# Performance work log

Hardware: AMD Instinct MI355X
Metric: run time of the kernel (lower is better)

The kernel has to match this reference:

```python
import jax, jax.numpy as jnp
import numpy as np

B, S, D_IN = 2, 2048, 1024
DIM, H, G = 64, 16, 4  # head dim, num_heads, kv groups


def setup_inputs() -> dict:
    key = jax.random.key(0)
    ks = jax.random.split(key, 9)
    query = jax.random.normal(ks[0], (B, S, D_IN), dtype=jnp.float32)
    key_t = jax.random.normal(ks[1], (B, S, D_IN), dtype=jnp.float32)
    value = jax.random.normal(ks[2], (B, S, D_IN), dtype=jnp.float32)
    # causal mask; masked_fill where mask == 0
    mask = jnp.tril(jnp.ones((S, S), dtype=jnp.int32))[None]  # [1,S,S]
    sc = 1.0 / np.sqrt(D_IN)
    Wq = jax.random.normal(ks[3], (H, D_IN, DIM), dtype=jnp.float32) * sc
    bq = jnp.zeros((H, DIM), dtype=jnp.float32)
    Wk = jax.random.normal(ks[4], (G, D_IN, DIM), dtype=jnp.float32) * sc
    bk = jnp.zeros((G, DIM), dtype=jnp.float32)
    Wv = jax.random.normal(ks[5], (G, D_IN, DIM), dtype=jnp.float32) * sc
    bv = jnp.zeros((G, DIM), dtype=jnp.float32)
    return {"query": query, "key": key_t, "value": value, "mask": mask,
            "Wq": Wq, "bq": bq, "Wk": Wk, "bk": bk, "Wv": Wv, "bv": bv}


def reference(query, key, value, mask, Wq, bq, Wk, bk, Wv, bv):
    # batched per-head projections (replaces the Python loop over heads)
    Q = jnp.einsum('bsd,hde->bhse', query, Wq) + bq[None, :, None, :]   # [B,H,S,E]
    K = jnp.einsum('bsd,gde->bgse', key, Wk) + bk[None, :, None, :]     # [B,G,S,E]
    V = jnp.einsum('bsd,gde->bgse', value, Wv) + bv[None, :, None, :]   # [B,G,S,E]
    # head i uses KV group i % G (as in the original loop)
    g_idx = jnp.arange(H) % G
    Kh = K[:, g_idx]  # [B,H,S,E]
    Vh = V[:, g_idx]
    attn = jnp.einsum('bhqe,bhke->bhqk', Q, Kh) / np.sqrt(DIM)          # [B,H,S,S]
    attn = jnp.where(mask[:, None] == 0, jnp.float32(-1e9), attn)
    p = jax.nn.softmax(attn, axis=-1)
    z = jnp.einsum('bhqk,bhke->bhqe', p, Vh)                             # [B,H,S,E]
    # concat heads along last dim (same order as torch.cat of z_list)
    return z.transpose(0, 2, 1, 3).reshape(B, S, H * DIM)
```

## Files before the change

### kernel.cpp

```cpp
#include <hip/hip_runtime.h>
#include <hip/hip_bf16.h>
#include <math.h>

#define S_LEN 2048
#define DIN   1024
#define NH    16
#define NG    4

typedef short s16x8 __attribute__((ext_vector_type(8)));
typedef float f32x4 __attribute__((ext_vector_type(4)));

__device__ __forceinline__ unsigned short f2bf(float x) {
  union { float f; unsigned u; } v; v.f = x;
  unsigned r = v.u + 0x7FFFu + ((v.u >> 16) & 1u);
  return (unsigned short)(r >> 16);
}
__device__ __forceinline__ unsigned cvtpk(float a, float b) {
  unsigned r;
  asm("v_cvt_pk_bf16_f32 %0, %1, %2" : "=v"(r) : "v"(a), "v"(b));
  return r;
}


__global__ __launch_bounds__(256) void k_cast(
    const float* __restrict__ q, const float* __restrict__ k,
    const float* __restrict__ v, unsigned short* __restrict__ AF) {
  const float* src = (blockIdx.y == 0) ? q : (blockIdx.y == 1) ? k : v;
  unsigned short* dst = AF + (size_t)blockIdx.y * 4194304;
  int flat = blockIdx.x * 256 + threadIdx.x;
  int b = flat >> 18, s = (flat >> 7) & 2047, d0 = (flat & 127) * 8;
  const float* sp = src + (size_t)(b * 2048 + s) * 1024 + d0;
  float4 x = *(const float4*)sp;
  float4 y = *(const float4*)(sp + 4);
  union { s16x8 v; unsigned u[4]; } r;
  r.u[0] = cvtpk(x.x, x.y); r.u[1] = cvtpk(x.z, x.w);
  r.u[2] = cvtpk(y.x, y.y); r.u[3] = cvtpk(y.z, y.w);
  unsigned short* p = dst + (size_t)((b * 128 + (s >> 4)) * 32 + (d0 >> 5)) * 512
                    + (s & 15) * 8 + ((d0 >> 3) & 3) * 128;
  *(s16x8*)p = r.v;
}

__global__ __launch_bounds__(256) void k_wtrans(
    const float* __restrict__ Wq, const float* __restrict__ Wk,
    const float* __restrict__ Wv, unsigned short* __restrict__ WF) {
  __shared__ __align__(16) unsigned short T[64][72];
  const int u = blockIdx.x >> 4, D0 = (blockIdx.x & 15) * 64;
  const int t = threadIdx.x;
  const float* src = (u < 16) ? (Wq + (size_t)u * 65536)
                   : (u < 20) ? (Wk + (size_t)(u - 16) * 65536)
                              : (Wv + (size_t)(u - 20) * 65536);
  const int e4 = (t & 15) * 4, dl = t >> 4;
  #pragma unroll
  for (int p = 0; p < 4; ++p) {
    const int d = p * 16 + dl;
    float4 v = *(const float4*)(src + (size_t)(D0 + d) * 64 + e4);
    T[e4 + 0][d] = f2bf(v.x); T[e4 + 1][d] = f2bf(v.y);
    T[e4 + 2][d] = f2bf(v.z); T[e4 + 3][d] = f2bf(v.w);
  }
  __syncthreads();
  const int j = t & 7;
  #pragma unroll
  for (int p = 0; p < 2; ++p) {
    const int e = p * 32 + (t >> 3);
    unsigned short* dst = WF + (size_t)u * 65536
        + (size_t)((e >> 4) * 32 + (D0 >> 5) + (j >> 2)) * 512
        + (e & 15) * 8 + (j & 3) * 128;
    *(s16x8*)dst = *(const s16x8*)&T[e][j * 8];
  }
}

__global__ __launch_bounds__(256, 4) void k_project(
    const unsigned short* __restrict__ AF,
    const float* __restrict__ bq, const float* __restrict__ bk,
    const float* __restrict__ bv,
    const unsigned short* __restrict__ WF,
    unsigned short* __restrict__ QF,
    unsigned short* __restrict__ KF,
    unsigned short* __restrict__ VF) {
  const int i = blockIdx.x;
  const int lid = (i & 7) * 96 + (i >> 3);
  const int strip = lid / 48;
  const int rr = lid % 48;
  const int b = rr / 24, u = rr % 24;
  const int tid = threadIdx.x;
  const int w = tid >> 6, lane = tid & 63, lq = lane & 15, gq = lane >> 4;

  const unsigned short* AFp = AF
      + (size_t)((u < 16) ? 0 : (u < 20) ? 1 : 2) * 4194304
      + (size_t)b * 2097152;
  const float* bias = (u < 16) ? bq + u * 64
                    : (u < 20) ? bk + (u - 16) * 64 : bv + (u - 20) * 64;
  const unsigned short* WFp = WF + (size_t)u * 65536;
  const int sb0 = strip * 8 + w * 2;
  const float OSC = (u < 16) ? 0.1803368801111204f : 1.0f;

  f32x4 acc[2][4] = {};
  s16x8 aE[2], bE[4], aO[2], bO[4];

  auto LD = [&](s16x8 (&a)[2], s16x8 (&bf)[4], int dk) {
    a[0] = *(const s16x8*)(AFp + (size_t)((sb0 + 0) * 32 + dk) * 512 + lane * 8);
    a[1] = *(const s16x8*)(AFp + (size_t)((sb0 + 1) * 32 + dk) * 512 + lane * 8);
    #pragma unroll
    for (int n = 0; n < 4; ++n)
      bf[n] = *(const s16x8*)(WFp + (size_t)(n * 32 + dk) * 512 + lane * 8);
  };
  auto FM = [&](const s16x8 (&a)[2], const s16x8 (&bf)[4]) {
    #pragma unroll
    for (int rf = 0; rf < 2; ++rf)
      #pragma unroll
      for (int n = 0; n < 4; ++n)
        acc[rf][n] = __builtin_amdgcn_mfma_f32_16x16x32_bf16(a[rf], bf[n], acc[rf][n], 0, 0, 0);
  };

  LD(aE, bE, 0);
  for (int dk = 0; dk < 32; dk += 2) {
    LD(aO, bO, dk + 1);
    FM(aE, bE);
    if (dk + 2 < 32) LD(aE, bE, dk + 2);
    FM(aO, bO);
  }

  float bvv[4];
  #pragma unroll
  for (int n = 0; n < 4; ++n) bvv[n] = bias[n * 16 + lq];

  unsigned short* dst = (u < 16) ? QF + (size_t)(b * 16 + u) * 131072
                      : (u < 20) ? KF + (size_t)(b * 4 + (u - 16)) * 131072
                                 : VF + (size_t)(b * 4 + (u - 20)) * 131072;
  #pragma unroll
  for (int rf = 0; rf < 2; ++rf)
    #pragma unroll
    for (int n = 0; n < 4; ++n)
      #pragma unroll
      for (int r = 0; r < 4; ++r) {
        const int s = strip * 128 + w * 32 + rf * 16 + gq * 4 + r;
        const int d = n * 16 + lq;
        const unsigned short hv = f2bf((acc[rf][n][r] + bvv[n]) * OSC);
        if (u < 20)
          dst[(size_t)((s >> 4) * 2 + (d >> 5)) * 512
              + (s & 15) * 8 + ((d >> 3) & 3) * 128 + (d & 7)] = hv;
        else
          dst[(size_t)(n * 64 + (s >> 5)) * 512
              + lq * 8 + ((s >> 3) & 3) * 128 + (s & 7)] = hv;
      }
}

__global__ __launch_bounds__(256, 3) void k_attn(
    const unsigned short* __restrict__ QF, const unsigned short* __restrict__ KF,
    const unsigned short* __restrict__ VF, float* __restrict__ out) {
  __shared__ __align__(16) unsigned short P[4][16][72];
  const int tid = threadIdx.x;
  const int w = tid >> 6, lane = tid & 63, lq = lane & 15, gq = lane >> 4;
  const int x = blockIdx.x;
  const int xcd = x & 7, li = x >> 3;
  const int g = xcd & 3;
  const int j = 127 - (li * 2 + (xcd >> 2));
  const int h = g + 4 * w;
  const int b = blockIdx.y;

  const unsigned short* QFp = QF + (size_t)(b * NH + h) * 131072;
  const unsigned short* KFp = KF + (size_t)(b * NG + g) * 131072;
  const unsigned short* VFp = VF + (size_t)(b * NG + g) * 131072;
  const int nt = (j >> 2) + 1;

  const s16x8 qf0 = *(const s16x8*)(QFp + (size_t)(j * 2 + 0) * 512 + lane * 8);
  const s16x8 qf1 = *(const s16x8*)(QFp + (size_t)(j * 2 + 1) * 512 + lane * 8);
  f32x4 z[4] = {};
  float lsum = 0.f;

  auto loadK = [&](s16x8 (&A)[4], s16x8 (&B)[4], int t) {
    #pragma unroll
    for (int f = 0; f < 4; ++f) {
      const unsigned short* kp = KFp + (size_t)((t * 4 + f) * 2) * 512 + lane * 8;
      A[f] = *(const s16x8*)kp;
      B[f] = *(const s16x8*)(kp + 512);
    }
  };

  auto tile = [&](const s16x8 (&kA)[4], const s16x8 (&kB)[4], int t) {
    const int k0 = t * 64;
    s16x8 vb[4][2];
    #pragma unroll
    for (int n = 0; n < 4; ++n)
      #pragma unroll
      for (int ks = 0; ks < 2; ++ks)
        vb[n][ks] = *(const s16x8*)(VFp + (size_t)(n * 64 + t * 2 + ks) * 512 + lane * 8);
    f32x4 sv[4];
    __builtin_amdgcn_s_setprio(1);
    #pragma unroll
    for (int f = 0; f < 4; ++f) {
      f32x4 s = {};
      s = __builtin_amdgcn_mfma_f32_16x16x32_bf16(kA[f], qf0, s, 0, 0, 0);
      s = __builtin_amdgcn_mfma_f32_16x16x32_bf16(kB[f], qf1, s, 0, 0, 0);
      sv[f] = s;
    }
    __builtin_amdgcn_s_setprio(0);
    if (t == nt - 1) {
      const int qrow = j * 16 + lq;
      #pragma unroll
      for (int f = 0; f < 4; ++f)
        #pragma unroll
        for (int r = 0; r < 4; ++r)
          if (k0 + f * 16 + gq * 4 + r > qrow) sv[f][r] = -1e30f;
    }
    float s0 = 0.f, s1 = 0.f;
    #pragma unroll
    for (int f = 0; f < 4; ++f) {
      float p0 = __builtin_amdgcn_exp2f(sv[f][0]);
      float p1 = __builtin_amdgcn_exp2f(sv[f][1]);
      float p2 = __builtin_amdgcn_exp2f(sv[f][2]);
      float p3 = __builtin_amdgcn_exp2f(sv[f][3]);
      s0 += p0 + p1; s1 += p2 + p3;
      *(uint2*)&P[w][lq][f * 16 + gq * 4] = make_uint2(cvtpk(p0, p1), cvtpk(p2, p3));
    }
    lsum += s0 + s1;
    s16x8 pa[2];
    #pragma unroll
    for (int ks = 0; ks < 2; ++ks)
      pa[ks] = *(const s16x8*)&P[w][lq][ks * 32 + gq * 8];
    __builtin_amdgcn_s_setprio(1);
    #pragma unroll
    for (int n = 0; n < 4; ++n)
      #pragma unroll
      for (int ks = 0; ks < 2; ++ks)
        z[n] = __builtin_amdgcn_mfma_f32_16x16x32_bf16(pa[ks], vb[n][ks], z[n], 0, 0, 0);
    __builtin_amdgcn_s_setprio(0);
  };

  s16x8 cA[4], cB[4], nA[4], nB[4];
  loadK(cA, cB, 0);
  int t = 0;
  while (true) {
    loadK(nA, nB, (t + 1 < nt) ? t + 1 : t);
    tile(cA, cB, t);
    if (++t >= nt) break;
    loadK(cA, cB, (t + 1 < nt) ? t + 1 : t);
    tile(nA, nB, t);
    if (++t >= nt) break;
  }

  lsum += __shfl_xor(lsum, 16);
  lsum += __shfl_xor(lsum, 32);
  float* outp = out + (size_t)b * S_LEN * 1024 + h * 64;
  #pragma unroll
  for (int r = 0; r < 4; ++r) {
    float lr = __shfl(lsum, gq * 4 + r, 64);
    float inv = __builtin_amdgcn_rcpf(lr);
    float* op = outp + (size_t)(j * 16 + gq * 4 + r) * 1024;
    #pragma unroll
    for (int n = 0; n < 4; ++n) op[n * 16 + lq] = z[n][r] * inv;
  }
}

extern "C" void kernel_launch(void* const* d_in, const int* in_sizes, int n_in,
                              void* d_out, int out_size, void* d_ws, size_t ws_size,
                              hipStream_t stream) {
  const float* query = (const float*)d_in[0];
  const float* key   = (const float*)d_in[1];
  const float* value = (const float*)d_in[2];
  const float* Wq = (const float*)d_in[4];
  const float* bq = (const float*)d_in[5];
  const float* Wk = (const float*)d_in[6];
  const float* bk = (const float*)d_in[7];
  const float* Wv = (const float*)d_in[8];
  const float* bv = (const float*)d_in[9];
  float* out = (float*)d_out;

  unsigned short* AF = (unsigned short*)d_ws;
  unsigned short* WF = AF + 12582912;
  unsigned short* QF = WF + 1572864;
  unsigned short* KF = QF + 4194304;
  unsigned short* VF = KF + 1048576;

  hipLaunchKernelGGL(k_cast, dim3(2048, 3), dim3(256), 0, stream,
                     query, key, value, AF);
  hipLaunchKernelGGL(k_wtrans, dim3(384), dim3(256), 0, stream, Wq, Wk, Wv, WF);
  hipLaunchKernelGGL(k_project, dim3(768), dim3(256), 0, stream,
                     AF, bq, bk, bv, WF, QF, KF, VF);
  hipLaunchKernelGGL(k_attn, dim3(512, 2), dim3(256), 0, stream, QF, KF, VF, out);
}
```

Before: 90.92 us.

## Stage shared K/V tiles in LDS via global_load_lds double buffering

In the attention kernel, each of the four waves now loads a quarter of each K and V tile straight into a double-buffered shared-memory region with global_load_lds, instead of every wave fetching the full tiles into registers. The four heads in a block share one KV group, so this cuts redundant global and L2 traffic by four and frees the registers that held K/V. The cost is a block-wide barrier with vmcnt(0) on every tile, extra LDS reads, and dropping the occupancy hint from launch bounds.

```diff
diff --git a/kernel.cpp b/kernel.cpp
--- a/kernel.cpp
+++ b/kernel.cpp
@@ -20,6 +20,11 @@
   asm("v_cvt_pk_bf16_f32 %0, %1, %2" : "=v"(r) : "v"(a), "v"(b));
   return r;
 }
+
+#define GLOAD_LDS16(gsrc, ldst)                                              \
+  __builtin_amdgcn_global_load_lds(                                         \
+      (const __attribute__((address_space(1))) unsigned int*)(gsrc),        \
+      (__attribute__((address_space(3))) unsigned int*)(ldst), 16, 0, 0)
 
 
 __global__ __launch_bounds__(256) void k_cast(
@@ -145,9 +150,10 @@
       }
 }
 
-__global__ __launch_bounds__(256, 3) void k_attn(
+__global__ __launch_bounds__(256) void k_attn(
     const unsigned short* __restrict__ QF, const unsigned short* __restrict__ KF,
     const unsigned short* __restrict__ VF, float* __restrict__ out) {
+  __shared__ __align__(16) unsigned short KV[2][8192];
   __shared__ __align__(16) unsigned short P[4][16][72];
   const int tid = threadIdx.x;
   const int w = tid >> 6, lane = tid & 63, lq = lane & 15, gq = lane >> 4;
@@ -168,34 +174,34 @@
   f32x4 z[4] = {};
   float lsum = 0.f;
 
-  auto loadK = [&](s16x8 (&A)[4], s16x8 (&B)[4], int t) {
-    #pragma unroll
-    for (int f = 0; f < 4; ++f) {
-      const unsigned short* kp = KFp + (size_t)((t * 4 + f) * 2) * 512 + lane * 8;
-      A[f] = *(const s16x8*)kp;
-      B[f] = *(const s16x8*)(kp + 512);
-    }
-  };
-
-  auto tile = [&](const s16x8 (&kA)[4], const s16x8 (&kB)[4], int t) {
-    const int k0 = t * 64;
-    s16x8 vb[4][2];
-    #pragma unroll
-    for (int n = 0; n < 4; ++n)
-      #pragma unroll
-      for (int ks = 0; ks < 2; ++ks)
-        vb[n][ks] = *(const s16x8*)(VFp + (size_t)(n * 64 + t * 2 + ks) * 512 + lane * 8);
+  auto stage = [&](int t, int buf) {
+    const unsigned short* ks = KFp + (size_t)t * 4096 + (w * 2) * 512 + lane * 8;
+    unsigned short* kd = &KV[buf][(w * 2) * 512];
+    GLOAD_LDS16(ks, kd);
+    GLOAD_LDS16(ks + 512, kd + 512);
+    const unsigned short* vs = VFp + (size_t)(w * 64 + t * 2) * 512 + lane * 8;
+    unsigned short* vd = &KV[buf][4096 + (w * 2) * 512];
+    GLOAD_LDS16(vs, vd);
+    GLOAD_LDS16(vs + 512, vd + 512);
+  };
+
+  auto tile = [&](int t, int buf) {
+    const unsigned short* kb = &KV[buf][0];
+    const unsigned short* vb = &KV[buf][4096];
     f32x4 sv[4];
     __builtin_amdgcn_s_setprio(1);
     #pragma unroll
     for (int f = 0; f < 4; ++f) {
+      const s16x8 kA = *(const s16x8*)(kb + (f * 2 + 0) * 512 + lane * 8);
+      const s16x8 kB = *(const s16x8*)(kb + (f * 2 + 1) * 512 + lane * 8);
       f32x4 s = {};
-      s = __builtin_amdgcn_mfma_f32_16x16x32_bf16(kA[f], qf0, s, 0, 0, 0);
-      s = __builtin_amdgcn_mfma_f32_16x16x32_bf16(kB[f], qf1, s, 0, 0, 0);
+      s = __builtin_amdgcn_mfma_f32_16x16x32_bf16(kA, qf0, s, 0, 0, 0);
+      s = __builtin_amdgcn_mfma_f32_16x16x32_bf16(kB, qf1, s, 0, 0, 0);
       sv[f] = s;
     }
     __builtin_amdgcn_s_setprio(0);
     if (t == nt - 1) {
+      const int k0 = t * 64;
       const int qrow = j * 16 + lq;
       #pragma unroll
       for (int f = 0; f < 4; ++f)
@@ -214,29 +220,29 @@
       *(uint2*)&P[w][lq][f * 16 + gq * 4] = make_uint2(cvtpk(p0, p1), cvtpk(p2, p3));
     }
     lsum += s0 + s1;
-    s16x8 pa[2];
-    #pragma unroll
-    for (int ks = 0; ks < 2; ++ks)
-      pa[ks] = *(const s16x8*)&P[w][lq][ks * 32 + gq * 8];
+    const s16x8 pa0 = *(const s16x8*)&P[w][lq][gq * 8];
+    const s16x8 pa1 = *(const s16x8*)&P[w][lq][32 + gq * 8];
     __builtin_amdgcn_s_setprio(1);
     #pragma unroll
-    for (int n = 0; n < 4; ++n)
-      #pragma unroll
-      for (int ks = 0; ks < 2; ++ks)
-        z[n] = __builtin_amdgcn_mfma_f32_16x16x32_bf16(pa[ks], vb[n][ks], z[n], 0, 0, 0);
+    for (int n = 0; n < 4; ++n) {
+      const s16x8 v0 = *(const s16x8*)(vb + (n * 2 + 0) * 512 + lane * 8);
+      const s16x8 v1 = *(const s16x8*)(vb + (n * 2 + 1) * 512 + lane * 8);
+      z[n] = __builtin_amdgcn_mfma_f32_16x16x32_bf16(pa0, v0, z[n], 0, 0, 0);
+      z[n] = __builtin_amdgcn_mfma_f32_16x16x32_bf16(pa1, v1, z[n], 0, 0, 0);
+    }
     __builtin_amdgcn_s_setprio(0);
   };
 
-  s16x8 cA[4], cB[4], nA[4], nB[4];
-  loadK(cA, cB, 0);
-  int t = 0;
-  while (true) {
-    loadK(nA, nB, (t + 1 < nt) ? t + 1 : t);
-    tile(cA, cB, t);
-    if (++t >= nt) break;
-    loadK(cA, cB, (t + 1 < nt) ? t + 1 : t);
-    tile(nA, nB, t);
-    if (++t >= nt) break;
+  stage(0, 0);
+  asm volatile("s_waitcnt vmcnt(0)");
+  __syncthreads();
+  int buf = 0;
+  for (int t = 0; t < nt; ++t) {
+    if (t + 1 < nt) stage(t + 1, buf ^ 1);
+    tile(t, buf);
+    asm volatile("s_waitcnt vmcnt(0)");
+    __syncthreads();
+    buf ^= 1;
   }
 
   lsum += __shfl_xor(lsum, 16);
```

Result: faster. 86.91 us (-4.4%).
